# Kernel tuning notes

Hardware: AMD Instinct MI355X
Metric: run time of the kernel (lower is better)

Reference implementation:

```python
import jax, jax.numpy as jnp
import numpy as np

N = 50000      # nodes
E = 800000     # edges (before self-loops)
F_IN = 128     # num_features
H = 4          # heads
C = 64         # hidden_channels
HC = H * C     # 256
NEG_SLOPE = 0.2


def setup_inputs() -> dict:
    key = jax.random.key(0)
    ks = jax.random.split(key, 20)
    x = jax.random.normal(ks[0], (N, F_IN), dtype=jnp.float32)
    edge_index = jax.random.randint(ks[1], (2, E), 0, N, dtype=jnp.int32)
    s = 0.05
    inp = {"x": x, "edge_index": edge_index}
    dims_in = [F_IN, HC, HC, HC]
    for l in range(4):
        kW, ka, kb = jax.random.split(ks[2 + l], 3)
        inp[f"W{l+1}"] = jax.random.normal(kW, (dims_in[l], HC), dtype=jnp.float32) * s
        inp[f"a_src{l+1}"] = jax.random.normal(ka, (H, C), dtype=jnp.float32) * s
        inp[f"a_dst{l+1}"] = jax.random.normal(kb, (H, C), dtype=jnp.float32) * s
        inp[f"b{l+1}"] = jnp.zeros((HC,), dtype=jnp.float32)
    return inp


def gat_conv(x, src, dst, W, a_src, a_dst, b):
    # x: [N, F_in] -> h: [N, H, C]
    h = (x @ W).reshape(N, H, C)
    es = jnp.sum(h * a_src, axis=-1)  # [N, H] per-node source logits
    ed = jnp.sum(h * a_dst, axis=-1)  # [N, H]
    e = jax.nn.leaky_relu(es[src] + ed[dst], NEG_SLOPE)  # [Etot, H]
    m = jax.ops.segment_max(e, dst, num_segments=N)      # per-dst max
    m = jnp.where(jnp.isfinite(m), m, 0.0)
    ex = jnp.exp(e - m[dst])
    denom = jax.ops.segment_sum(ex, dst, num_segments=N)
    alpha = ex / (denom[dst] + 1e-16)                     # edge softmax
    out = jax.ops.segment_sum(alpha[:, :, None] * h[src], dst, num_segments=N)
    return out.reshape(N, HC) + b


def reference(x, edge_index,
              W1, a_src1, a_dst1, b1,
              W2, a_src2, a_dst2, b2,
              W3, a_src3, a_dst3, b3,
              W4, a_src4, a_dst4, b4):
    loop = jnp.arange(N, dtype=edge_index.dtype)
    src = jnp.concatenate([edge_index[0], loop])  # add self-loops (PyG default)
    dst = jnp.concatenate([edge_index[1], loop])
    x1 = jax.nn.relu(gat_conv(x, src, dst, W1, a_src1, a_dst1, b1))
    x2 = jax.nn.relu(gat_conv(x1, src, dst, W2, a_src2, a_dst2, b2))
    x3 = jax.nn.relu(gat_conv(x2 + x1, src, dst, W3, a_src3, a_dst3, b3))
    x4 = jax.nn.relu(gat_conv(x2 + x3, src, dst, W4, a_src4, a_dst4, b4))
    # NOTE: source code calls conv4 again (not conv5) -- reproduced faithfully
    x5 = gat_conv(x4 + x3, src, dst, W4, a_src4, a_dst4, b4)
    return x5
```

## Files before the change

### kernel.cpp

```cpp
#include <hip/hip_runtime.h>
#include <hip/hip_bf16.h>

#define N_NODES 50000
#define E_EDGES 800000
#define ETOT (E_EDGES + N_NODES)
#define HC 256
#define NHEAD 4
#define CHAN 64
#define NEG 0.2f
#define NBLK ((N_NODES + 1023) / 1024)

typedef _Float16 half8 __attribute__((ext_vector_type(8)));
typedef _Float16 half4v __attribute__((ext_vector_type(4)));
typedef float float4v __attribute__((ext_vector_type(4)));


__global__ void count_kernel(const int* __restrict__ ei, int* __restrict__ counts) {
    int i = blockIdx.x * blockDim.x + threadIdx.x;
    if (i >= ETOT) return;
    int dst = (i < E_EDGES) ? ei[E_EDGES + i] : (i - E_EDGES);
    atomicAdd(&counts[dst], 1);
}

__global__ __launch_bounds__(256) void blocksum_kernel(const int* __restrict__ counts,
                                                       int* __restrict__ blocksums) {
    __shared__ int s[4];
    int b = blockIdx.x, tid = threadIdx.x;
    int base = b * 1024;
    int sum = 0;
    #pragma unroll
    for (int r = 0; r < 4; ++r) {
        int idx = base + r * 256 + tid;
        sum += (idx < N_NODES) ? counts[idx] : 0;
    }
    #pragma unroll
    for (int m = 1; m < 64; m <<= 1) sum += __shfl_xor(sum, m, 64);
    if ((tid & 63) == 0) s[tid >> 6] = sum;
    __syncthreads();
    if (tid == 0) blocksums[b] = s[0] + s[1] + s[2] + s[3];
}

__global__ __launch_bounds__(64) void blockscan_kernel(int* __restrict__ blocksums) {
    int tid = threadIdx.x;
    int v = (tid < NBLK) ? blocksums[tid] : 0;
    #pragma unroll
    for (int off = 1; off < 64; off <<= 1) {
        int t = __shfl_up(v, off, 64);
        if (tid >= off) v += t;
    }
    if (tid < NBLK) blocksums[tid] = v;
}

__global__ __launch_bounds__(1024) void scatter_scan_kernel(const int* __restrict__ counts,
                                                            const int* __restrict__ blocksums,
                                                            int* __restrict__ offsets,
                                                            int* __restrict__ cursor) {
    __shared__ int s[1024];
    int b = blockIdx.x, tid = threadIdx.x;
    int idx = b * 1024 + tid;
    int v = (idx < N_NODES) ? counts[idx] : 0;
    s[tid] = v;
    __syncthreads();
    for (int off = 1; off < 1024; off <<= 1) {
        int t = (tid >= off) ? s[tid - off] : 0;
        __syncthreads();
        s[tid] += t;
        __syncthreads();
    }
    int excl = s[tid] - v + (b > 0 ? blocksums[b - 1] : 0);
    if (idx < N_NODES) { offsets[idx] = excl; cursor[idx] = excl; }
    if (idx == N_NODES - 1) offsets[N_NODES] = excl + v;
}

__global__ void fill_kernel(const int* __restrict__ ei, int* __restrict__ cursor,
                            int* __restrict__ csr_src) {
    int i = blockIdx.x * blockDim.x + threadIdx.x;
    if (i >= ETOT) return;
    int src, dst;
    if (i < E_EDGES) { src = ei[i]; dst = ei[E_EDGES + i]; }
    else             { src = i - E_EDGES; dst = src; }
    int pos = atomicAdd(&cursor[dst], 1);
    csr_src[pos] = src;
}


__global__ void wsplit_kernel(const float* __restrict__ W, _Float16* __restrict__ Wth,
                              _Float16* __restrict__ Wtl, int K) {
    int id = blockIdx.x * 256 + threadIdx.x;
    if (id >= K * 256) return;
    int n = id & 255, k = id >> 8;
    float w = W[(size_t)k * 256 + n];
    _Float16 h = (_Float16)w;
    _Float16 l = (_Float16)(w - (float)h);
    Wth[(size_t)n * K + k] = h;
    Wtl[(size_t)n * K + k] = l;
}


#define LDK 40

__global__ __launch_bounds__(256) void gemm_mfma_kernel(
        const float* __restrict__ A1, const float* __restrict__ A2,
        const _Float16* __restrict__ Wth, const _Float16* __restrict__ Wtl,
        _Float16* __restrict__ H16, int M, int K) {
    __shared__ _Float16 Ah[64][LDK];
    __shared__ _Float16 Al[64][LDK];
    __shared__ _Float16 Bh[256][LDK];
    __shared__ _Float16 Bl[256][LDK];

    int tid = threadIdx.x;
    int m0 = blockIdx.x * 64;
    int w = tid >> 6, lane = tid & 63;
    int rn = w * 64;
    int fr = lane & 15;
    int fk = (lane >> 4) * 8;

    int ar = tid >> 3;
    int ak = (tid & 7) * 4;
    int wr = tid >> 2;
    int wk = (tid & 3) * 8;

    float4v acc[4][4];
    #pragma unroll
    for (int i = 0; i < 4; ++i)
        #pragma unroll
        for (int j = 0; j < 4; ++j)
            acc[i][j] = (float4v){0.f, 0.f, 0.f, 0.f};

    for (int k0 = 0; k0 < K; k0 += 32) {
        __syncthreads();
        #pragma unroll
        for (int g = 0; g < 2; ++g) {
            int r = g * 32 + ar;
            int row = m0 + r;
            float4 v = make_float4(0.f, 0.f, 0.f, 0.f);
            if (row < M) {
                v = *(const float4*)(A1 + (size_t)row * K + k0 + ak);
                if (A2) {
                    float4 u = *(const float4*)(A2 + (size_t)row * K + k0 + ak);
                    v.x += u.x; v.y += u.y; v.z += u.z; v.w += u.w;
                }
            }
            half4v hv = {(_Float16)v.x, (_Float16)v.y, (_Float16)v.z, (_Float16)v.w};
            half4v lv = {(_Float16)(v.x - (float)hv[0]), (_Float16)(v.y - (float)hv[1]),
                         (_Float16)(v.z - (float)hv[2]), (_Float16)(v.w - (float)hv[3])};
            *(half4v*)&Ah[r][ak] = hv;
            *(half4v*)&Al[r][ak] = lv;
        }
        #pragma unroll
        for (int g = 0; g < 4; ++g) {
            int r = g * 64 + wr;
            *(half8*)&Bh[r][wk] = *(const half8*)(Wth + (size_t)r * K + k0 + wk);
            *(half8*)&Bl[r][wk] = *(const half8*)(Wtl + (size_t)r * K + k0 + wk);
        }
        __syncthreads();
        half8 afh[4], afl[4], bfh[4], bfl[4];
        #pragma unroll
        for (int t = 0; t < 4; ++t) {
            afh[t] = *(const half8*)&Ah[t * 16 + fr][fk];
            afl[t] = *(const half8*)&Al[t * 16 + fr][fk];
            bfh[t] = *(const half8*)&Bh[rn + t * 16 + fr][fk];
            bfl[t] = *(const half8*)&Bl[rn + t * 16 + fr][fk];
        }
        #pragma unroll
        for (int tm = 0; tm < 4; ++tm)
            #pragma unroll
            for (int tn = 0; tn < 4; ++tn) {
                float4v c = acc[tm][tn];
                c = __builtin_amdgcn_mfma_f32_16x16x32_f16(afl[tm], bfh[tn], c, 0, 0, 0);
                c = __builtin_amdgcn_mfma_f32_16x16x32_f16(afh[tm], bfl[tn], c, 0, 0, 0);
                c = __builtin_amdgcn_mfma_f32_16x16x32_f16(afh[tm], bfh[tn], c, 0, 0, 0);
                acc[tm][tn] = c;
            }
    }
    #pragma unroll
    for (int tm = 0; tm < 4; ++tm) {
        int rbase = m0 + tm * 16 + (lane >> 4) * 4;
        #pragma unroll
        for (int i = 0; i < 4; ++i) {
            int row = rbase + i;
            if (row < M) {
                #pragma unroll
                for (int tn = 0; tn < 4; ++tn)
                    H16[(size_t)row * HC + rn + tn * 16 + fr] = (_Float16)acc[tm][tn][i];
            }
        }
    }
}


__global__ __launch_bounds__(256) void esed_kernel(const _Float16* __restrict__ H16,
                                                   const float* __restrict__ a_src,
                                                   const float* __restrict__ a_dst,
                                                   float* __restrict__ es, float* __restrict__ ed) {
    int tid = threadIdx.x;
    int lane = tid & 63;
    int node = blockIdx.x * 4 + (tid >> 6);
    int head = lane >> 4;
    int cc = (lane & 15) * 4;
    half4v hv = *(const half4v*)(H16 + (size_t)node * HC + lane * 4);
    float4 h4 = make_float4((float)hv[0], (float)hv[1], (float)hv[2], (float)hv[3]);
    float4 as = *(const float4*)(a_src + head * CHAN + cc);
    float4 ad = *(const float4*)(a_dst + head * CHAN + cc);
    float ps = h4.x * as.x + h4.y * as.y + h4.z * as.z + h4.w * as.w;
    float pd = h4.x * ad.x + h4.y * ad.y + h4.z * ad.z + h4.w * ad.w;
    #pragma unroll
    for (int m = 1; m < 16; m <<= 1) {
        ps += __shfl_xor(ps, m, 64);
        pd += __shfl_xor(pd, m, 64);
    }
    if ((lane & 15) == 0) {
        es[node * NHEAD + head] = ps;
        ed[node * NHEAD + head] = pd;
    }
}


__global__ __launch_bounds__(256) void gat_aggregate_kernel(
        const _Float16* __restrict__ H16, const float* __restrict__ es, const float* __restrict__ ed,
        const int* __restrict__ offsets, const int* __restrict__ csr_src,
        const float* __restrict__ bias, float* __restrict__ out, int do_relu) {
    __shared__ float alpha_lds[4][256];
    int tid = threadIdx.x;
    int w = tid >> 6, lane = tid & 63;
    int n = blockIdx.x * 4 + w;
    int off = offsets[n];
    int deg = offsets[n + 1] - off;
    float4 edv = *(const float4*)(ed + (size_t)n * 4);

    if (deg <= 64) {
        int sreg = 0;
        float4 e4 = make_float4(-1e30f, -1e30f, -1e30f, -1e30f);
        if (lane < deg) {
            sreg = csr_src[off + lane];
            float4 esv = *(const float4*)(es + (size_t)sreg * 4);
            e4.x = esv.x + edv.x; e4.y = esv.y + edv.y;
            e4.z = esv.z + edv.z; e4.w = esv.w + edv.w;
            e4.x = (e4.x > 0.f) ? e4.x : NEG * e4.x;
            e4.y = (e4.y > 0.f) ? e4.y : NEG * e4.y;
            e4.z = (e4.z > 0.f) ? e4.z : NEG * e4.z;
            e4.w = (e4.w > 0.f) ? e4.w : NEG * e4.w;
        }
        float4 m4 = e4;
        #pragma unroll
        for (int msk = 1; msk < 64; msk <<= 1) {
            m4.x = fmaxf(m4.x, __shfl_xor(m4.x, msk, 64));
            m4.y = fmaxf(m4.y, __shfl_xor(m4.y, msk, 64));
            m4.z = fmaxf(m4.z, __shfl_xor(m4.z, msk, 64));
            m4.w = fmaxf(m4.w, __shfl_xor(m4.w, msk, 64));
        }
        float4 ex4 = make_float4(0.f, 0.f, 0.f, 0.f);
        if (lane < deg) {
            ex4.x = __expf(e4.x - m4.x); ex4.y = __expf(e4.y - m4.y);
            ex4.z = __expf(e4.z - m4.z); ex4.w = __expf(e4.w - m4.w);
        }
        float4 l4 = ex4;
        #pragma unroll
        for (int msk = 1; msk < 64; msk <<= 1) {
            l4.x += __shfl_xor(l4.x, msk, 64);
            l4.y += __shfl_xor(l4.y, msk, 64);
            l4.z += __shfl_xor(l4.z, msk, 64);
            l4.w += __shfl_xor(l4.w, msk, 64);
        }
        float4 a4;
        a4.x = ex4.x / (l4.x + 1e-16f);
        a4.y = ex4.y / (l4.y + 1e-16f);
        a4.z = ex4.z / (l4.z + 1e-16f);
        a4.w = ex4.w / (l4.w + 1e-16f);
        *(float4*)&alpha_lds[w][lane * 4] = a4;

        int hl = lane & 31, side = lane >> 5;
        int hd = hl >> 3;
        float av[8] = {0.f, 0.f, 0.f, 0.f, 0.f, 0.f, 0.f, 0.f};
        #pragma unroll 2
        for (int j = side; j < deg; j += 2) {
            int s = __shfl(sreg, j, 64);
            float al = alpha_lds[w][j * 4 + hd];
            half8 hv = *(const half8*)(H16 + (size_t)s * HC + hl * 8);
            #pragma unroll
            for (int c = 0; c < 8; ++c) av[c] += al * (float)hv[c];
        }
        #pragma unroll
        for (int c = 0; c < 8; ++c) av[c] += __shfl_xor(av[c], 32, 64);
        if (side == 0) {
            float4 b0 = *(const float4*)(bias + hl * 8);
            float4 b1 = *(const float4*)(bias + hl * 8 + 4);
            float4 o0 = make_float4(av[0] + b0.x, av[1] + b0.y, av[2] + b0.z, av[3] + b0.w);
            float4 o1 = make_float4(av[4] + b1.x, av[5] + b1.y, av[6] + b1.z, av[7] + b1.w);
            if (do_relu) {
                o0.x = fmaxf(o0.x, 0.f); o0.y = fmaxf(o0.y, 0.f);
                o0.z = fmaxf(o0.z, 0.f); o0.w = fmaxf(o0.w, 0.f);
                o1.x = fmaxf(o1.x, 0.f); o1.y = fmaxf(o1.y, 0.f);
                o1.z = fmaxf(o1.z, 0.f); o1.w = fmaxf(o1.w, 0.f);
            }
            *(float4*)(out + (size_t)n * HC + hl * 8) = o0;
            *(float4*)(out + (size_t)n * HC + hl * 8 + 4) = o1;
        }
        return;
    }

    int head = lane >> 4;
    float4 acc0 = make_float4(0.f, 0.f, 0.f, 0.f);
    float m[4] = {-1e30f, -1e30f, -1e30f, -1e30f};
    float l[4] = {0.f, 0.f, 0.f, 0.f};
    for (int base = 0; base < deg; base += 64) {
        int j = base + lane;
        if (j < deg) {
            int s = csr_src[off + j];
            float4 esv = *(const float4*)(es + (size_t)s * 4);
            float e[4] = {esv.x + edv.x, esv.y + edv.y, esv.z + edv.z, esv.w + edv.w};
            #pragma unroll
            for (int h = 0; h < 4; ++h) {
                e[h] = (e[h] > 0.f) ? e[h] : NEG * e[h];
                float M2 = fmaxf(m[h], e[h]);
                l[h] = l[h] * __expf(m[h] - M2) + __expf(e[h] - M2);
                m[h] = M2;
            }
        }
    }
    #pragma unroll
    for (int msk = 1; msk < 64; msk <<= 1) {
        #pragma unroll
        for (int h = 0; h < 4; ++h) {
            float mo = __shfl_xor(m[h], msk, 64);
            float lo = __shfl_xor(l[h], msk, 64);
            float M2 = fmaxf(m[h], mo);
            l[h] = l[h] * __expf(m[h] - M2) + lo * __expf(mo - M2);
            m[h] = M2;
        }
    }
    float fm = m[head];
    float fr = 1.f / (l[head] + 1e-16f);
    float edh = ((const float*)&edv)[head];
    for (int j = 0; j < deg; ++j) {
        int s = csr_src[off + j];
        float e = es[(size_t)s * 4 + head] + edh;
        e = (e > 0.f) ? e : NEG * e;
        float alpha = __expf(e - fm) * fr;
        half4v h0 = *(const half4v*)(H16 + (size_t)s * HC + lane * 4);
        acc0.x += alpha * (float)h0[0]; acc0.y += alpha * (float)h0[1];
        acc0.z += alpha * (float)h0[2]; acc0.w += alpha * (float)h0[3];
    }
    float4 b4 = *(const float4*)(bias + lane * 4);
    float4 o;
    o.x = acc0.x + b4.x; o.y = acc0.y + b4.y;
    o.z = acc0.z + b4.z; o.w = acc0.w + b4.w;
    if (do_relu) {
        o.x = fmaxf(o.x, 0.f); o.y = fmaxf(o.y, 0.f);
        o.z = fmaxf(o.z, 0.f); o.w = fmaxf(o.w, 0.f);
    }
    *(float4*)(out + (size_t)n * HC + lane * 4) = o;
}


extern "C" void kernel_launch(void* const* d_in, const int* in_sizes, int n_in,
                              void* d_out, int out_size, void* d_ws, size_t ws_size,
                              hipStream_t stream) {
    const float* x  = (const float*)d_in[0];
    const int*   ei = (const int*)d_in[1];
    const float *W[5], *Asrc[5], *Adst[5], *Bs[5];
    for (int l = 0; l < 4; ++l) {
        W[l]    = (const float*)d_in[2 + l * 4];
        Asrc[l] = (const float*)d_in[3 + l * 4];
        Adst[l] = (const float*)d_in[4 + l * 4];
        Bs[l]   = (const float*)d_in[5 + l * 4];
    }
    W[4] = W[3]; Asrc[4] = Asrc[3]; Adst[4] = Adst[3]; Bs[4] = Bs[3];

    char* ws = (char*)d_ws;
    size_t off = 0;
    auto alloc = [&](size_t bytes) -> void* {
        void* p = ws + off;
        off += (bytes + 255) & ~(size_t)255;
        return p;
    };
    _Float16* h16  = (_Float16*)alloc((size_t)N_NODES * HC * 2);
    float* xa      = (float*)alloc((size_t)N_NODES * HC * 4);
    float* xb      = (float*)alloc((size_t)N_NODES * HC * 4);
    float* xc      = (float*)alloc((size_t)N_NODES * HC * 4);
    float* es      = (float*)alloc((size_t)N_NODES * 4 * 4);
    float* ed      = (float*)alloc((size_t)N_NODES * 4 * 4);
    int*   counts  = (int*)alloc((size_t)N_NODES * 4);
    int*   offsets = (int*)alloc((size_t)(N_NODES + 1) * 4);
    int*   cursor  = (int*)alloc((size_t)N_NODES * 4);
    int*   csr_src = (int*)alloc((size_t)ETOT * 4);
    int*   blocksums = (int*)alloc((size_t)NBLK * 4);
    _Float16 *Wth[5], *Wtl[5];
    int Ks[4] = {128, 256, 256, 256};
    for (int l = 0; l < 4; ++l) {
        Wth[l] = (_Float16*)alloc((size_t)256 * Ks[l] * 2);
        Wtl[l] = (_Float16*)alloc((size_t)256 * Ks[l] * 2);
    }
    Wth[4] = Wth[3]; Wtl[4] = Wtl[3];

    hipMemsetAsync(counts, 0, (size_t)N_NODES * 4, stream);
    count_kernel<<<(ETOT + 255) / 256, 256, 0, stream>>>(ei, counts);
    blocksum_kernel<<<NBLK, 256, 0, stream>>>(counts, blocksums);
    blockscan_kernel<<<1, 64, 0, stream>>>(blocksums);
    scatter_scan_kernel<<<NBLK, 1024, 0, stream>>>(counts, blocksums, offsets, cursor);
    fill_kernel<<<(ETOT + 255) / 256, 256, 0, stream>>>(ei, cursor, csr_src);
    for (int l = 0; l < 4; ++l)
        wsplit_kernel<<<(Ks[l] * 256 + 255) / 256, 256, 0, stream>>>(W[l], Wth[l], Wtl[l], Ks[l]);

    auto layer = [&](const float* in1, const float* in2, int K, int l, float* outp, int relu) {
        gemm_mfma_kernel<<<(N_NODES + 63) / 64, 256, 0, stream>>>(in1, in2, Wth[l], Wtl[l],
                                                                  h16, N_NODES, K);
        esed_kernel<<<N_NODES / 4, 256, 0, stream>>>(h16, Asrc[l], Adst[l], es, ed);
        gat_aggregate_kernel<<<N_NODES / 4, 256, 0, stream>>>(h16, es, ed, offsets, csr_src,
                                                              Bs[l], outp, relu);
    };

    float* out = (float*)d_out;
    layer(x,  nullptr, 128, 0, xa, 1);
    layer(xa, nullptr, 256, 1, xb, 1);
    layer(xb, xa,      256, 2, xc, 1);
    layer(xb, xc,      256, 3, xa, 1);
    layer(xa, xc,      256, 4, out, 0);
}
```

Before: 887.4 us.

## Fuse attention-logit computation into GEMM epilogue and prefetch next K tile

```diff
diff --git a/kernel.cpp b/kernel.cpp
--- a/kernel.cpp
+++ b/kernel.cpp
@@ -102,7 +102,9 @@
 __global__ __launch_bounds__(256) void gemm_mfma_kernel(
         const float* __restrict__ A1, const float* __restrict__ A2,
         const _Float16* __restrict__ Wth, const _Float16* __restrict__ Wtl,
-        _Float16* __restrict__ H16, int M, int K) {
+        const float* __restrict__ a_src, const float* __restrict__ a_dst,
+        _Float16* __restrict__ H16, float* __restrict__ es, float* __restrict__ ed,
+        int M, int K) {
     __shared__ _Float16 Ah[64][LDK];
     __shared__ _Float16 Al[64][LDK];
     __shared__ _Float16 Bh[256][LDK];
@@ -113,7 +115,8 @@
     int w = tid >> 6, lane = tid & 63;
     int rn = w * 64;
     int fr = lane & 15;
-    int fk = (lane >> 4) * 8;
+    int q  = lane >> 4;
+    int fk = q * 8;
 
     int ar = tid >> 3;
     int ak = (tid & 7) * 4;
@@ -127,20 +130,37 @@
         for (int j = 0; j < 4; ++j)
             acc[i][j] = (float4v){0.f, 0.f, 0.f, 0.f};
 
+    bool has2 = (A2 != nullptr);
+    float4 pa1[2], pa2[2];
+    half8 pbh[4], pbl[4];
+
+    auto load_tile = [&](int k0) {
+        #pragma unroll
+        for (int g = 0; g < 2; ++g) {
+            int row = m0 + g * 32 + ar;
+            pa1[g] = make_float4(0.f, 0.f, 0.f, 0.f);
+            pa2[g] = make_float4(0.f, 0.f, 0.f, 0.f);
+            if (row < M) {
+                pa1[g] = *(const float4*)(A1 + (size_t)row * K + k0 + ak);
+                if (has2) pa2[g] = *(const float4*)(A2 + (size_t)row * K + k0 + ak);
+            }
+        }
+        #pragma unroll
+        for (int g = 0; g < 4; ++g) {
+            int r = g * 64 + wr;
+            pbh[g] = *(const half8*)(Wth + (size_t)r * K + k0 + wk);
+            pbl[g] = *(const half8*)(Wtl + (size_t)r * K + k0 + wk);
+        }
+    };
+
+    load_tile(0);
     for (int k0 = 0; k0 < K; k0 += 32) {
-        __syncthreads();
         #pragma unroll
         for (int g = 0; g < 2; ++g) {
             int r = g * 32 + ar;
-            int row = m0 + r;
-            float4 v = make_float4(0.f, 0.f, 0.f, 0.f);
-            if (row < M) {
-                v = *(const float4*)(A1 + (size_t)row * K + k0 + ak);
-                if (A2) {
-                    float4 u = *(const float4*)(A2 + (size_t)row * K + k0 + ak);
-                    v.x += u.x; v.y += u.y; v.z += u.z; v.w += u.w;
-                }
-            }
+            float4 v;
+            v.x = pa1[g].x + pa2[g].x; v.y = pa1[g].y + pa2[g].y;
+            v.z = pa1[g].z + pa2[g].z; v.w = pa1[g].w + pa2[g].w;
             half4v hv = {(_Float16)v.x, (_Float16)v.y, (_Float16)v.z, (_Float16)v.w};
             half4v lv = {(_Float16)(v.x - (float)hv[0]), (_Float16)(v.y - (float)hv[1]),
                          (_Float16)(v.z - (float)hv[2]), (_Float16)(v.w - (float)hv[3])};
@@ -150,10 +170,11 @@
         #pragma unroll
         for (int g = 0; g < 4; ++g) {
             int r = g * 64 + wr;
-            *(half8*)&Bh[r][wk] = *(const half8*)(Wth + (size_t)r * K + k0 + wk);
-            *(half8*)&Bl[r][wk] = *(const half8*)(Wtl + (size_t)r * K + k0 + wk);
+            *(half8*)&Bh[r][wk] = pbh[g];
+            *(half8*)&Bl[r][wk] = pbl[g];
         }
         __syncthreads();
+        if (k0 + 32 < K) load_tile(k0 + 32);
         half8 afh[4], afl[4], bfh[4], bfl[4];
         #pragma unroll
         for (int t = 0; t < 4; ++t) {
@@ -172,46 +193,39 @@
                 c = __builtin_amdgcn_mfma_f32_16x16x32_f16(afh[tm], bfh[tn], c, 0, 0, 0);
                 acc[tm][tn] = c;
             }
+        __syncthreads();
+    }
+
+    float asv[4], adv[4];
+    #pragma unroll
+    for (int tn = 0; tn < 4; ++tn) {
+        asv[tn] = a_src[w * CHAN + tn * 16 + fr];
+        adv[tn] = a_dst[w * CHAN + tn * 16 + fr];
     }
     #pragma unroll
     for (int tm = 0; tm < 4; ++tm) {
-        int rbase = m0 + tm * 16 + (lane >> 4) * 4;
         #pragma unroll
         for (int i = 0; i < 4; ++i) {
-            int row = rbase + i;
-            if (row < M) {
-                #pragma unroll
-                for (int tn = 0; tn < 4; ++tn)
-                    H16[(size_t)row * HC + rn + tn * 16 + fr] = (_Float16)acc[tm][tn][i];
-            }
-        }
-    }
-}
-
-
-__global__ __launch_bounds__(256) void esed_kernel(const _Float16* __restrict__ H16,
-                                                   const float* __restrict__ a_src,
-                                                   const float* __restrict__ a_dst,
-                                                   float* __restrict__ es, float* __restrict__ ed) {
-    int tid = threadIdx.x;
-    int lane = tid & 63;
-    int node = blockIdx.x * 4 + (tid >> 6);
-    int head = lane >> 4;
-    int cc = (lane & 15) * 4;
-    half4v hv = *(const half4v*)(H16 + (size_t)node * HC + lane * 4);
-    float4 h4 = make_float4((float)hv[0], (float)hv[1], (float)hv[2], (float)hv[3]);
-    float4 as = *(const float4*)(a_src + head * CHAN + cc);
-    float4 ad = *(const float4*)(a_dst + head * CHAN + cc);
-    float ps = h4.x * as.x + h4.y * as.y + h4.z * as.z + h4.w * as.w;
-    float pd = h4.x * ad.x + h4.y * ad.y + h4.z * ad.z + h4.w * ad.w;
-    #pragma unroll
-    for (int m = 1; m < 16; m <<= 1) {
-        ps += __shfl_xor(ps, m, 64);
-        pd += __shfl_xor(pd, m, 64);
-    }
-    if ((lane & 15) == 0) {
-        es[node * NHEAD + head] = ps;
-        ed[node * NHEAD + head] = pd;
+            int row = m0 + tm * 16 + q * 4 + i;
+            float ps = 0.f, pd = 0.f;
+            #pragma unroll
+            for (int tn = 0; tn < 4; ++tn) {
+                float hv = acc[tm][tn][i];
+                ps += hv * asv[tn];
+                pd += hv * adv[tn];
+                if (row < M)
+                    H16[(size_t)row * HC + rn + tn * 16 + fr] = (_Float16)hv;
+            }
+            #pragma unroll
+            for (int msk = 1; msk < 16; msk <<= 1) {
+                ps += __shfl_xor(ps, msk, 64);
+                pd += __shfl_xor(pd, msk, 64);
+            }
+            if (fr == 0 && row < M) {
+                es[row * NHEAD + w] = ps;
+                ed[row * NHEAD + w] = pd;
+            }
+        }
     }
 }
 
@@ -330,13 +344,13 @@
         }
     }
     float fm = m[head];
-    float fr = 1.f / (l[head] + 1e-16f);
+    float fr2 = 1.f / (l[head] + 1e-16f);
     float edh = ((const float*)&edv)[head];
     for (int j = 0; j < deg; ++j) {
         int s = csr_src[off + j];
         float e = es[(size_t)s * 4 + head] + edh;
         e = (e > 0.f) ? e : NEG * e;
-        float alpha = __expf(e - fm) * fr;
+        float alpha = __expf(e - fm) * fr2;
         half4v h0 = *(const half4v*)(H16 + (size_t)s * HC + lane * 4);
         acc0.x += alpha * (float)h0[0]; acc0.y += alpha * (float)h0[1];
         acc0.z += alpha * (float)h0[2]; acc0.w += alpha * (float)h0[3];
@@ -403,9 +417,8 @@
         wsplit_kernel<<<(Ks[l] * 256 + 255) / 256, 256, 0, stream>>>(W[l], Wth[l], Wtl[l], Ks[l]);
 
     auto layer = [&](const float* in1, const float* in2, int K, int l, float* outp, int relu) {
-        gemm_mfma_kernel<<<(N_NODES + 63) / 64, 256, 0, stream>>>(in1, in2, Wth[l], Wtl[l],
-                                                                  h16, N_NODES, K);
-        esed_kernel<<<N_NODES / 4, 256, 0, stream>>>(h16, Asrc[l], Adst[l], es, ed);
+        gemm_mfma_kernel<<<(N_NODES + 63) / 64, 256, 0, stream>>>(
+            in1, in2, Wth[l], Wtl[l], Asrc[l], Adst[l], h16, es, ed, N_NODES, K);
         gat_aggregate_kernel<<<N_NODES / 4, 256, 0, stream>>>(h16, es, ed, offsets, csr_src,
                                                               Bs[l], outp, relu);
     };
```

Measured after the change: 811.2 us. -8.6%, faster.
